# Kernel tuning notes

Measured on AMD Instinct MI355X. Metric: run time of the kernel, lower is better.

Reference implementation:

```python
import jax, jax.numpy as jnp
import numpy as np
from jax import lax

B, C_IN, D, H, W = 1, 64, 48, 48, 48
R = 3
PC = 64          # proj_channels
OC = 128         # out_channels
K = (2 * R + 1) ** 3  # 343 offsets
OFFSETS = np.array([(dz, dy, dx)
                    for dz in range(-R, R + 1)
                    for dy in range(-R, R + 1)
                    for dx in range(-R, R + 1)], dtype=np.int32)


def setup_inputs() -> dict:
    key = jax.random.key(0)
    ks = jax.random.split(key, 10)
    s = 0.05
    return {
        'source_features': jax.random.normal(ks[0], (B, C_IN, D, H, W), jnp.float32),
        'warped_target_features': jax.random.normal(ks[1], (B, C_IN, D, H, W), jnp.float32),
        'proj_src_w': jax.random.normal(ks[2], (PC, C_IN, 1, 1, 1), jnp.float32) * s,
        'proj_src_b': jax.random.normal(ks[3], (PC,), jnp.float32) * s,
        'proj_tgt_w': jax.random.normal(ks[4], (PC, C_IN, 1, 1, 1), jnp.float32) * s,
        'proj_tgt_b': jax.random.normal(ks[5], (PC,), jnp.float32) * s,
        'enc1_w': jax.random.normal(ks[6], (OC, K + 3, 3, 3, 3), jnp.float32) * s,
        'enc1_b': jax.random.normal(ks[7], (OC,), jnp.float32) * s,
        'enc2_w': jax.random.normal(ks[8], (OC, OC, 3, 3, 3), jnp.float32) * s,
        'enc2_b': jax.random.normal(ks[9], (OC,), jnp.float32) * s,
    }


def conv3d(x, w, b, pad):
    out = lax.conv_general_dilated(
        x, w, window_strides=(1, 1, 1), padding=[(pad, pad)] * 3,
        dimension_numbers=('NCDHW', 'OIDHW', 'NCDHW'))
    return out + b[None, :, None, None, None]


def l2norm_c(x):
    # torch F.normalize(dim=1): x / max(||x||_2, 1e-12)
    n = jnp.sqrt(jnp.sum(x * x, axis=1, keepdims=True))
    return x / jnp.maximum(n, 1e-12)


def instance_norm(x, eps=1e-5):
    # InstanceNorm3d, affine=False: per (B,C), biased var over D,H,W
    m = jnp.mean(x, axis=(2, 3, 4), keepdims=True)
    v = jnp.var(x, axis=(2, 3, 4), keepdims=True)
    return (x - m) * lax.rsqrt(v + eps)


def reference(source_features, warped_target_features,
              proj_src_w, proj_src_b, proj_tgt_w, proj_tgt_b,
              enc1_w, enc1_b, enc2_w, enc2_b):
    sp = l2norm_c(conv3d(source_features, proj_src_w, proj_src_b, 0))
    tp = l2norm_c(conv3d(warped_target_features, proj_tgt_w, proj_tgt_b, 0))
    padded = jnp.pad(tp, ((0, 0), (0, 0), (R, R), (R, R), (R, R)), mode='edge')
    offs = jnp.asarray(OFFSETS)  # [K,3] int32

    def corr_one(off):
        # shifted window of padded target, dot over channels -> [B,D,H,W]
        shifted = lax.dynamic_slice(
            padded, (0, 0, R + off[0], R + off[1], R + off[2]), sp.shape)
        return jnp.sum(sp * shifted, axis=1)

    corr = lax.map(corr_one, offs)          # [K,B,D,H,W]
    corr = jnp.moveaxis(corr, 0, 1)         # [B,K,D,H,W]

    # online-softmax expected offset == softmax over K weighted by offset vecs
    wts = jax.nn.softmax(corr, axis=1)
    eo = jnp.einsum('bkdhw,kc->bcdhw', wts, offs.astype(sp.dtype))  # [B,3,D,H,W]

    feat = jnp.concatenate([corr, eo], axis=1)  # [B,K+3,D,H,W]
    h = conv3d(feat, enc1_w, enc1_b, 1)
    h = jax.nn.gelu(instance_norm(h), approximate=False)
    h = conv3d(h, enc2_w, enc2_b, 1)
    h = jax.nn.gelu(instance_norm(h), approximate=False)
    return h
```

## Files before the change

### kernel.cpp

```cpp
#include <hip/hip_runtime.h>
#include <math.h>
#include <stdint.h>

#define VOL 110592
#define CINP 64
#define PCH 64

typedef short short8 __attribute__((ext_vector_type(8)));
typedef float floatx4 __attribute__((ext_vector_type(4)));
typedef _Float16 h8 __attribute__((ext_vector_type(8)));
typedef _Float16 h2v __attribute__((ext_vector_type(2)));

__device__ __forceinline__ ushort f2bf(float f) {
    union { float f; uint32_t u; } v; v.f = f;
    uint32_t r = v.u + 0x7FFFu + ((v.u >> 16) & 1u);
    return (ushort)(r >> 16);
}

__device__ __forceinline__ float hdot2(h2v a, h2v b, float c) {
#if __has_builtin(__builtin_amdgcn_fdot2)
    return __builtin_amdgcn_fdot2(a, b, c, false);
#else
    return fmaf((float)a[0], (float)b[0], fmaf((float)a[1], (float)b[1], c));
#endif
}

__global__ __launch_bounds__(256) void proj_l2norm_kernel(
    const float* __restrict__ x,
    const float* __restrict__ w,
    const float* __restrict__ b,
    _Float16* __restrict__ out)
{
    const int v = blockIdx.x * 256 + threadIdx.x;
    float xr[CINP];
    for (int ci = 0; ci < CINP; ci++)
        xr[ci] = x[(size_t)ci * VOL + v];

    float acc[PCH];
    for (int c = 0; c < PCH; c++) {
        float a = b[c];
        #pragma unroll
        for (int ci = 0; ci < CINP; ci++)
            a = fmaf(w[c * CINP + ci], xr[ci], a);
        acc[c] = a;
    }
    float s = 0.f;
    #pragma unroll
    for (int c = 0; c < PCH; c++) s += acc[c] * acc[c];
    const float inv = 1.0f / fmaxf(sqrtf(s), 1e-12f);
    #pragma unroll
    for (int c = 0; c < PCH; c++)
        out[(size_t)v * PCH + c] = (_Float16)(acc[c] * inv);
}

__global__ __launch_bounds__(256) void corr_fused_kernel(
    const _Float16* __restrict__ sp,
    const _Float16* __restrict__ tp,
    ushort* __restrict__ featT)
{
    const int t  = threadIdx.x;
    const int c8 = t & 7;
    const int vg = t >> 3;
    const int v  = blockIdx.x * 32 + vg;
    const int x = v % 48, y = (v / 48) % 48, z = v / 2304;

    __shared__ __align__(16) ushort lds[32 * 360];

    const h8 s = *(const h8*)(sp + (size_t)v * PCH + c8 * 8);

    const bool owner = (c8 < 7);
    const float fdx_own = (float)(c8 - 3);
    float ssum = 0.f, e0 = 0.f, e1 = 0.f;

    int k = 0;
    for (int dz = -3; dz <= 3; dz++) {
        const int zb = min(max(z + dz, 0), 47) * 2304;
        const float fdz = (float)dz;
        for (int dy = -3; dy <= 3; dy++) {
            const int rb = zb + min(max(y + dy, 0), 47) * 48;
            const float fdy = (float)dy;
            h8 tv[7];
            #pragma unroll
            for (int dxi = 0; dxi < 7; dxi++) {
                const int xc = min(max(x + dxi - 3, 0), 47);
                tv[dxi] = *(const h8*)(tp + (size_t)(rb + xc) * PCH + c8 * 8);
            }
            float p[8];
            #pragma unroll
            for (int dxi = 0; dxi < 7; dxi++) {
                const h8 tvv = tv[dxi];
                float d0 = hdot2((h2v){s[0], s[1]}, (h2v){tvv[0], tvv[1]}, 0.f);
                d0 = hdot2((h2v){s[2], s[3]}, (h2v){tvv[2], tvv[3]}, d0);
                float d1 = hdot2((h2v){s[4], s[5]}, (h2v){tvv[4], tvv[5]}, 0.f);
                d1 = hdot2((h2v){s[6], s[7]}, (h2v){tvv[6], tvv[7]}, d1);
                p[dxi] = d0 + d1;
            }
            p[7] = 0.f;

            float r0, r1, r2, r3;
            {
                const bool hi = (c8 & 1);
                float m0 = hi ? p[0] : p[1];
                float m1 = hi ? p[2] : p[3];
                float m2 = hi ? p[4] : p[5];
                float m3 = hi ? p[6] : p[7];
                m0 = __shfl_xor(m0, 1);
                m1 = __shfl_xor(m1, 1);
                m2 = __shfl_xor(m2, 1);
                m3 = __shfl_xor(m3, 1);
                r0 = (hi ? p[1] : p[0]) + m0;
                r1 = (hi ? p[3] : p[2]) + m1;
                r2 = (hi ? p[5] : p[4]) + m2;
                r3 = (hi ? p[7] : p[6]) + m3;
            }
            float q0, q1;
            {
                const bool hi = (c8 & 2);
                float m0 = hi ? r0 : r1;
                float m1 = hi ? r2 : r3;
                m0 = __shfl_xor(m0, 2);
                m1 = __shfl_xor(m1, 2);
                q0 = (hi ? r1 : r0) + m0;
                q1 = (hi ? r3 : r2) + m1;
            }
            float dot;
            {
                const bool hi = (c8 & 4);
                float m0 = hi ? q0 : q1;
                m0 = __shfl_xor(m0, 4);
                dot = (hi ? q1 : q0) + m0;
            }

            if (owner) {
                lds[vg * 360 + k + c8] = f2bf(dot);
                const float e = __expf(dot);
                ssum += e;
                e0 = fmaf(e, fdz, e0);
                e1 = fmaf(e, fdy, e1);
            }
            k += 7;
        }
    }

    float e2 = fdx_own * ssum;
    #pragma unroll
    for (int m = 1; m < 8; m <<= 1) {
        ssum += __shfl_xor(ssum, m);
        e0   += __shfl_xor(e0, m);
        e1   += __shfl_xor(e1, m);
        e2   += __shfl_xor(e2, m);
    }

    if (c8 == 0) {
        const float inv = 1.f / ssum;
        lds[vg * 360 + 343] = f2bf(e0 * inv);
        lds[vg * 360 + 344] = f2bf(e1 * inv);
        lds[vg * 360 + 345] = f2bf(e2 * inv);
        #pragma unroll
        for (int j = 346; j < 352; j++) lds[vg * 360 + j] = 0;
    }
    __syncthreads();

    ushort* ob = featT + (size_t)blockIdx.x * 32 * 352;
    #pragma unroll
    for (int j = 0; j < 6; j++) {
        const int idx = t + j * 256;
        if (idx < 1408) {
            const int row = idx / 44, col = (idx % 44) * 8;
            *(int4*)(ob + (size_t)row * 352 + col) = *(const int4*)(&lds[row * 360 + col]);
        }
    }
}

template<int CIN, int CPAD>
__global__ __launch_bounds__(256) void wprep_kernel(
    const float* __restrict__ w, ushort* __restrict__ wTo, float* __restrict__ zp)
{
    if (blockIdx.x == 0 && threadIdx.x < 4) zp[threadIdx.x] = 0.f;
    const int oc = blockIdx.x;
    for (int idx = threadIdx.x; idx < CPAD * 27; idx += 256) {
        const int icp = idx / 27, tap = idx - icp * 27;
        float val = 0.f;
        if (icp < CIN) val = w[((size_t)oc * CIN + icp) * 27 + tap];
        wTo[((size_t)tap * 128 + oc) * CPAD + icp] = f2bf(val);
    }
}

template<int CPAD>
__global__ __launch_bounds__(256, 4) void conv3_mfma_kernel(
    const ushort* __restrict__ xT,
    const ushort* __restrict__ wT,
    const float* __restrict__ bias,
    const ushort* __restrict__ zpad,
    float* __restrict__ out)
{
    const int blk = (blockIdx.x % 8) * 108 + (blockIdx.x / 8);
    const int tx = blk % 3, ty = (blk / 3) % 12, tz = blk / 36;
    const int x0 = tx * 16, y0 = ty * 4, z0 = tz * 2;
    const int t = threadIdx.x;
    const int wave = t >> 6;
    const int lane = t & 63;
    const int l = lane & 15;
    const int q = lane >> 4;
    const int ocw = (wave & 1) * 64;
    const int mzw = wave >> 1;

    __shared__ __align__(16) ushort win[432 * 32];

    int off[7];
    #pragma unroll
    for (int it = 0; it < 7; it++) {
        const int c = wave + it * 4;
        off[it] = -1;
        if (c < 27) {
            const int i = c * 64 + lane;
            const int p = i >> 2, g = i & 3;
            const int wz = p / 108, pr = p - wz * 108;
            const int wy = pr / 18, wx = pr - wy * 18;
            const int gz = z0 + wz - 1, gy = y0 + wy - 1, gx = x0 + wx - 1;
            if ((unsigned)gx < 48u && (unsigned)gy < 48u && (unsigned)gz < 48u)
                off[it] = ((gz * 2304 + gy * 48 + gx) * CPAD + g * 8) * 2;
        }
    }

    floatx4 acc[4][4];
    #pragma unroll
    for (int i = 0; i < 4; i++)
        #pragma unroll
        for (int j = 0; j < 4; j++)
            acc[i][j] = (floatx4){0.f, 0.f, 0.f, 0.f};

    const ushort* wbase = wT + (size_t)(ocw + l) * CPAD + q * 8;
    const int ldsbase = (mzw * 108 + l) * 32 + q * 8;

    const int NCH = CPAD / 32;
    #pragma unroll 1
    for (int ck = 0; ck < NCH; ck++) {
        if (ck) __syncthreads();

        const char* xck = (const char*)xT + (size_t)ck * 64;
        #pragma unroll
        for (int it = 0; it < 7; it++) {
            const int c = wave + it * 4;
            if (c < 27) {
                const ushort* gp = (off[it] >= 0)
                    ? (const ushort*)(xck + off[it])
                    : zpad;
                __builtin_amdgcn_global_load_lds(
                    (const __attribute__((address_space(1))) uint32_t*)gp,
                    (__attribute__((address_space(3))) uint32_t*)(win + c * 512 + lane * 8),
                    16, 0, 0);
            }
        }

        const ushort* wck = wbase + ck * 32;
        short8 A0[4], A1[4];
        A0[0] = *(const short8*)(wck);
        A0[1] = *(const short8*)(wck + 16 * CPAD);
        A0[2] = *(const short8*)(wck + 32 * CPAD);
        A0[3] = *(const short8*)(wck + 48 * CPAD);

        __syncthreads();

#define CONV_BODY(TP, AU, AL)                                              \
        {                                                                  \
            const int tpn_ = (TP) + 1;                                     \
            if (tpn_ < 27) {                                               \
                const ushort* wp_ = wck + (size_t)tpn_ * (128 * CPAD);     \
                AL[0] = *(const short8*)(wp_);                             \
                AL[1] = *(const short8*)(wp_ + 16 * CPAD);                 \
                AL[2] = *(const short8*)(wp_ + 32 * CPAD);                 \
                AL[3] = *(const short8*)(wp_ + 48 * CPAD);                 \
            }                                                              \
            const int dz_ = (TP) / 9;                                      \
            const int dy_ = ((TP) / 3) % 3;                                \
            const int dx_ = (TP) % 3;                                      \
            const int pb_ = ldsbase + (dz_ * 108 + dy_ * 18 + dx_) * 32;   \
            const short8 b0_ = *(const short8*)(&win[pb_ +    0]);         \
            const short8 b1_ = *(const short8*)(&win[pb_ +  576]);         \
            const short8 b2_ = *(const short8*)(&win[pb_ + 1152]);         \
            const short8 b3_ = *(const short8*)(&win[pb_ + 1728]);         \
            acc[0][0] = __builtin_amdgcn_mfma_f32_16x16x32_bf16(AU[0], b0_, acc[0][0], 0, 0, 0); \
            acc[1][0] = __builtin_amdgcn_mfma_f32_16x16x32_bf16(AU[1], b0_, acc[1][0], 0, 0, 0); \
            acc[2][0] = __builtin_amdgcn_mfma_f32_16x16x32_bf16(AU[2], b0_, acc[2][0], 0, 0, 0); \
            acc[3][0] = __builtin_amdgcn_mfma_f32_16x16x32_bf16(AU[3], b0_, acc[3][0], 0, 0, 0); \
            acc[0][1] = __builtin_amdgcn_mfma_f32_16x16x32_bf16(AU[0], b1_, acc[0][1], 0, 0, 0); \
            acc[1][1] = __builtin_amdgcn_mfma_f32_16x16x32_bf16(AU[1], b1_, acc[1][1], 0, 0, 0); \
            acc[2][1] = __builtin_amdgcn_mfma_f32_16x16x32_bf16(AU[2], b1_, acc[2][1], 0, 0, 0); \
            acc[3][1] = __builtin_amdgcn_mfma_f32_16x16x32_bf16(AU[3], b1_, acc[3][1], 0, 0, 0); \
            acc[0][2] = __builtin_amdgcn_mfma_f32_16x16x32_bf16(AU[0], b2_, acc[0][2], 0, 0, 0); \
            acc[1][2] = __builtin_amdgcn_mfma_f32_16x16x32_bf16(AU[1], b2_, acc[1][2], 0, 0, 0); \
            acc[2][2] = __builtin_amdgcn_mfma_f32_16x16x32_bf16(AU[2], b2_, acc[2][2], 0, 0, 0); \
            acc[3][2] = __builtin_amdgcn_mfma_f32_16x16x32_bf16(AU[3], b2_, acc[3][2], 0, 0, 0); \
            acc[0][3] = __builtin_amdgcn_mfma_f32_16x16x32_bf16(AU[0], b3_, acc[0][3], 0, 0, 0); \
            acc[1][3] = __builtin_amdgcn_mfma_f32_16x16x32_bf16(AU[1], b3_, acc[1][3], 0, 0, 0); \
            acc[2][3] = __builtin_amdgcn_mfma_f32_16x16x32_bf16(AU[2], b3_, acc[2][3], 0, 0, 0); \
            acc[3][3] = __builtin_amdgcn_mfma_f32_16x16x32_bf16(AU[3], b3_, acc[3][3], 0, 0, 0); \
        }

        #pragma unroll 1
        for (int tg = 0; tg < 13; tg++) {
            const int tp = tg * 2;
            CONV_BODY(tp, A0, A1);
            CONV_BODY(tp + 1, A1, A0);
        }
        CONV_BODY(26, A0, A1);
#undef CONV_BODY
    }

    #pragma unroll
    for (int nt = 0; nt < 4; nt++) {
        const int ocb = ocw + nt * 16 + q * 4;
        const float4 bv = *(const float4*)(bias + ocb);
        #pragma unroll
        for (int mt = 0; mt < 4; mt++) {
            const int v = (z0 + mzw) * 2304 + (y0 + mt) * 48 + x0 + l;
            out[(size_t)(ocb + 0) * VOL + v] = acc[nt][mt][0] + bv.x;
            out[(size_t)(ocb + 1) * VOL + v] = acc[nt][mt][1] + bv.y;
            out[(size_t)(ocb + 2) * VOL + v] = acc[nt][mt][2] + bv.z;
            out[(size_t)(ocb + 3) * VOL + v] = acc[nt][mt][3] + bv.w;
        }
    }
}

__global__ __launch_bounds__(256) void chan_stats_part_kernel(
    const float* __restrict__ x, float* __restrict__ pstats )
{
    const int c = blockIdx.x, g = blockIdx.y;
    const float4* p = (const float4*)(x + (size_t)c * VOL) + g * 3456;
    float s = 0.f, s2 = 0.f;
    #pragma unroll
    for (int j = 0; j < 14; j++) {
        const int i = threadIdx.x + j * 256;
        if (i < 3456) {
            const float4 v = p[i];
            s += v.x + v.y + v.z + v.w;
            s2 = fmaf(v.x, v.x, fmaf(v.y, v.y, fmaf(v.z, v.z, fmaf(v.w, v.w, s2))));
        }
    }
    s  += __shfl_down(s, 32);  s  += __shfl_down(s, 16);
    s  += __shfl_down(s, 8);   s  += __shfl_down(s, 4);
    s  += __shfl_down(s, 2);   s  += __shfl_down(s, 1);
    s2 += __shfl_down(s2, 32); s2 += __shfl_down(s2, 16);
    s2 += __shfl_down(s2, 8);  s2 += __shfl_down(s2, 4);
    s2 += __shfl_down(s2, 2);  s2 += __shfl_down(s2, 1);
    __shared__ float rs[4], rs2[4];
    if ((threadIdx.x & 63) == 0) {
        rs[threadIdx.x >> 6] = s;
        rs2[threadIdx.x >> 6] = s2;
    }
    __syncthreads();
    if (threadIdx.x == 0) {
        pstats[(c * 8 + g) * 2]     = rs[0] + rs[1] + rs[2] + rs[3];
        pstats[(c * 8 + g) * 2 + 1] = rs2[0] + rs2[1] + rs2[2] + rs2[3];
    }
}

__global__ __launch_bounds__(128) void chan_stats_fin_kernel(
    const float* __restrict__ pstats, float* __restrict__ stats )
{
    const int c = threadIdx.x;
    float s = 0.f, s2 = 0.f;
    #pragma unroll
    for (int g = 0; g < 8; g++) {
        s  += pstats[(c * 8 + g) * 2];
        s2 += pstats[(c * 8 + g) * 2 + 1];
    }
    const float mean = s / (float)VOL;
    const float var  = s2 / (float)VOL - mean * mean;
    stats[c * 2]     = mean;
    stats[c * 2 + 1] = rsqrtf(var + 1e-5f);
}

__device__ __forceinline__ float gelu_exact(float h)
{
    return 0.5f * h * (1.f + erff(h * 0.70710678118654752f));
}

__global__ __launch_bounds__(256) void norm_gelu_kernel(
    const float* __restrict__ x, const float* __restrict__ stats,
    float* __restrict__ out)
{
    const size_t i = (size_t)blockIdx.x * 256 + threadIdx.x;
    const int c = (int)(i / (VOL / 4));
    const float mean = stats[c * 2], rstd = stats[c * 2 + 1];
    const float4 xv = ((const float4*)x)[i];
    float4 o;
    o.x = gelu_exact((xv.x - mean) * rstd);
    o.y = gelu_exact((xv.y - mean) * rstd);
    o.z = gelu_exact((xv.z - mean) * rstd);
    o.w = gelu_exact((xv.w - mean) * rstd);
    ((float4*)out)[i] = o;
}

__global__ __launch_bounds__(256) void norm_gelu_transpose_kernel(
    const float* __restrict__ x, const float* __restrict__ stats,
    ushort* __restrict__ outT)
{
    __shared__ float tile[32][33];
    const int v0 = blockIdx.x * 32;
    const int c0 = blockIdx.y * 32;
    const int t = threadIdx.x;
    const int vl = t & 31, cl = t >> 5;
    #pragma unroll
    for (int i = 0; i < 4; i++) {
        const int c = c0 + cl + i * 8;
        const float mean = stats[c * 2], rstd = stats[c * 2 + 1];
        const float val = x[(size_t)c * VOL + v0 + vl];
        tile[cl + i * 8][vl] = gelu_exact((val - mean) * rstd);
    }
    __syncthreads();
    const int vw = t >> 3, cg = t & 7;
    ushort4 o;
    o.x = f2bf(tile[cg * 4 + 0][vw]);
    o.y = f2bf(tile[cg * 4 + 1][vw]);
    o.z = f2bf(tile[cg * 4 + 2][vw]);
    o.w = f2bf(tile[cg * 4 + 3][vw]);
    *(ushort4*)(outT + (size_t)(v0 + vw) * 128 + c0 + cg * 4) = o;
}

extern "C" void kernel_launch(void* const* d_in, const int* in_sizes, int n_in,
                              void* d_out, int out_size, void* d_ws, size_t ws_size,
                              hipStream_t stream)
{
    const float* src = (const float*)d_in[0];
    const float* tgt = (const float*)d_in[1];
    const float* psw = (const float*)d_in[2];
    const float* psb = (const float*)d_in[3];
    const float* ptw = (const float*)d_in[4];
    const float* ptb = (const float*)d_in[5];
    const float* e1w = (const float*)d_in[6];
    const float* e1b = (const float*)d_in[7];
    const float* e2w = (const float*)d_in[8];
    const float* e2b = (const float*)d_in[9];

    float* ws = (float*)d_ws;
    _Float16* sp  = (_Float16*)ws;
    _Float16* tp  = (_Float16*)(ws + (size_t)32 * VOL);
    ushort* featT = (ushort*)(ws + (size_t)128 * VOL);
    float*  h1    = ws;
    float*  h2    = ws + (size_t)128 * VOL;
    ushort* h1T   = (ushort*)(ws + (size_t)304 * VOL);
    float*  w1Tf  = ws + (size_t)368 * VOL;
    ushort* w1T   = (ushort*)w1Tf;
    float*  w2Tf  = w1Tf + 608256;
    ushort* w2T   = (ushort*)w2Tf;
    float*  stats = w2Tf + 221184;
    float*  pstats = stats + 256;
    float*  zpadf  = pstats + 2048;
    const ushort* zpad = (const ushort*)zpadf;

    wprep_kernel<346, 352><<<128, 256, 0, stream>>>(e1w, w1T, zpadf);
    wprep_kernel<128, 128><<<128, 256, 0, stream>>>(e2w, w2T, zpadf);

    proj_l2norm_kernel<<<432, 256, 0, stream>>>(src, psw, psb, sp);
    proj_l2norm_kernel<<<432, 256, 0, stream>>>(tgt, ptw, ptb, tp);
    corr_fused_kernel<<<3456, 256, 0, stream>>>(sp, tp, featT);

    conv3_mfma_kernel<352><<<864, 256, 0, stream>>>(featT, w1T, e1b, zpad, h1);
    chan_stats_part_kernel<<<dim3(128, 8), 256, 0, stream>>>(h1, pstats);
    chan_stats_fin_kernel<<<1, 128, 0, stream>>>(pstats, stats);
    norm_gelu_transpose_kernel<<<dim3(3456, 4), 256, 0, stream>>>(h1, stats, h1T);

    conv3_mfma_kernel<128><<<864, 256, 0, stream>>>(h1T, w2T, e2b, zpad, h2);
    chan_stats_part_kernel<<<dim3(128, 8), 256, 0, stream>>>(h2, pstats);
    chan_stats_fin_kernel<<<1, 128, 0, stream>>>(pstats, stats);
    norm_gelu_kernel<<<(128 * VOL) / 1024, 256, 0, stream>>>(h2, stats, (float*)d_out);
}
```

Measured before the change: 1.026 ms.

## Double-buffer LDS input window and prefetch B fragments in conv3 MFMA kernel

```diff
diff --git a/kernel.cpp b/kernel.cpp
--- a/kernel.cpp
+++ b/kernel.cpp
@@ -187,7 +187,7 @@
 }
 
 template<int CPAD>
-__global__ __launch_bounds__(256, 4) void conv3_mfma_kernel(
+__global__ __launch_bounds__(256, 2) void conv3_mfma_kernel(
     const ushort* __restrict__ xT,
     const ushort* __restrict__ wT,
     const float* __restrict__ bias,
@@ -205,7 +205,7 @@
     const int ocw = (wave & 1) * 64;
     const int mzw = wave >> 1;
 
-    __shared__ __align__(16) ushort win[432 * 32];
+    __shared__ __align__(16) ushort win[2][432 * 32];
 
     int off[7];
     #pragma unroll
@@ -233,36 +233,49 @@
     const ushort* wbase = wT + (size_t)(ocw + l) * CPAD + q * 8;
     const int ldsbase = (mzw * 108 + l) * 32 + q * 8;
 
+#define STAGE(CK, BUFP)                                                    \
+    {                                                                      \
+        const char* xck_ = (const char*)xT + (size_t)(CK) * 64;            \
+        _Pragma("unroll")                                                  \
+        for (int it_ = 0; it_ < 7; it_++) {                                \
+            const int c_ = wave + it_ * 4;                                 \
+            if (c_ < 27) {                                                 \
+                const ushort* gp_ = (off[it_] >= 0)                        \
+                    ? (const ushort*)(xck_ + off[it_]) : zpad;             \
+                __builtin_amdgcn_global_load_lds(                          \
+                    (const __attribute__((address_space(1))) uint32_t*)gp_,\
+                    (__attribute__((address_space(3))) uint32_t*)((BUFP) + c_ * 512 + lane * 8), \
+                    16, 0, 0);                                             \
+            }                                                              \
+        }                                                                  \
+    }
+
     const int NCH = CPAD / 32;
+
+    STAGE(0, &win[0][0]);
+    __syncthreads();
+
     #pragma unroll 1
     for (int ck = 0; ck < NCH; ck++) {
-        if (ck) __syncthreads();
-
-        const char* xck = (const char*)xT + (size_t)ck * 64;
-        #pragma unroll
-        for (int it = 0; it < 7; it++) {
-            const int c = wave + it * 4;
-            if (c < 27) {
-                const ushort* gp = (off[it] >= 0)
-                    ? (const ushort*)(xck + off[it])
-                    : zpad;
-                __builtin_amdgcn_global_load_lds(
-                    (const __attribute__((address_space(1))) uint32_t*)gp,
-                    (__attribute__((address_space(3))) uint32_t*)(win + c * 512 + lane * 8),
-                    16, 0, 0);
-            }
-        }
-
+        const ushort* cbuf = &win[ck & 1][0];
+        ushort* nbuf = &win[(ck + 1) & 1][0];
         const ushort* wck = wbase + ck * 32;
+
         short8 A0[4], A1[4];
         A0[0] = *(const short8*)(wck);
         A0[1] = *(const short8*)(wck + 16 * CPAD);
         A0[2] = *(const short8*)(wck + 32 * CPAD);
         A0[3] = *(const short8*)(wck + 48 * CPAD);
 
-        __syncthreads();
-
-#define CONV_BODY(TP, AU, AL)                                              \
+        short8 B0[4], B1[4];
+        B0[0] = *(const short8*)(&cbuf[ldsbase +    0]);
+        B0[1] = *(const short8*)(&cbuf[ldsbase +  576]);
+        B0[2] = *(const short8*)(&cbuf[ldsbase + 1152]);
+        B0[3] = *(const short8*)(&cbuf[ldsbase + 1728]);
+
+        if (ck + 1 < NCH) STAGE(ck + 1, nbuf);
+
+#define CONV_BODY(TP, AU, AL, BU, BL)                                      \
         {                                                                  \
             const int tpn_ = (TP) + 1;                                     \
             if (tpn_ < 27) {                                               \
@@ -271,42 +284,45 @@
                 AL[1] = *(const short8*)(wp_ + 16 * CPAD);                 \
                 AL[2] = *(const short8*)(wp_ + 32 * CPAD);                 \
                 AL[3] = *(const short8*)(wp_ + 48 * CPAD);                 \
+                const int dzn_ = tpn_ / 9;                                 \
+                const int dyn_ = (tpn_ / 3) % 3;                           \
+                const int dxn_ = tpn_ % 3;                                 \
+                const int pbn_ = ldsbase + (dzn_ * 108 + dyn_ * 18 + dxn_) * 32; \
+                BL[0] = *(const short8*)(&cbuf[pbn_ +    0]);              \
+                BL[1] = *(const short8*)(&cbuf[pbn_ +  576]);              \
+                BL[2] = *(const short8*)(&cbuf[pbn_ + 1152]);              \
+                BL[3] = *(const short8*)(&cbuf[pbn_ + 1728]);              \
             }                                                              \
-            const int dz_ = (TP) / 9;                                      \
-            const int dy_ = ((TP) / 3) % 3;                                \
-            const int dx_ = (TP) % 3;                                      \
-            const int pb_ = ldsbase + (dz_ * 108 + dy_ * 18 + dx_) * 32;   \
-            const short8 b0_ = *(const short8*)(&win[pb_ +    0]);         \
-            const short8 b1_ = *(const short8*)(&win[pb_ +  576]);         \
-            const short8 b2_ = *(const short8*)(&win[pb_ + 1152]);         \
-            const short8 b3_ = *(const short8*)(&win[pb_ + 1728]);         \
-            acc[0][0] = __builtin_amdgcn_mfma_f32_16x16x32_bf16(AU[0], b0_, acc[0][0], 0, 0, 0); \
-            acc[1][0] = __builtin_amdgcn_mfma_f32_16x16x32_bf16(AU[1], b0_, acc[1][0], 0, 0, 0); \
-            acc[2][0] = __builtin_amdgcn_mfma_f32_16x16x32_bf16(AU[2], b0_, acc[2][0], 0, 0, 0); \
-            acc[3][0] = __builtin_amdgcn_mfma_f32_16x16x32_bf16(AU[3], b0_, acc[3][0], 0, 0, 0); \
-            acc[0][1] = __builtin_amdgcn_mfma_f32_16x16x32_bf16(AU[0], b1_, acc[0][1], 0, 0, 0); \
-            acc[1][1] = __builtin_amdgcn_mfma_f32_16x16x32_bf16(AU[1], b1_, acc[1][1], 0, 0, 0); \
-            acc[2][1] = __builtin_amdgcn_mfma_f32_16x16x32_bf16(AU[2], b1_, acc[2][1], 0, 0, 0); \
-            acc[3][1] = __builtin_amdgcn_mfma_f32_16x16x32_bf16(AU[3], b1_, acc[3][1], 0, 0, 0); \
-            acc[0][2] = __builtin_amdgcn_mfma_f32_16x16x32_bf16(AU[0], b2_, acc[0][2], 0, 0, 0); \
-            acc[1][2] = __builtin_amdgcn_mfma_f32_16x16x32_bf16(AU[1], b2_, acc[1][2], 0, 0, 0); \
-            acc[2][2] = __builtin_amdgcn_mfma_f32_16x16x32_bf16(AU[2], b2_, acc[2][2], 0, 0, 0); \
-            acc[3][2] = __builtin_amdgcn_mfma_f32_16x16x32_bf16(AU[3], b2_, acc[3][2], 0, 0, 0); \
-            acc[0][3] = __builtin_amdgcn_mfma_f32_16x16x32_bf16(AU[0], b3_, acc[0][3], 0, 0, 0); \
-            acc[1][3] = __builtin_amdgcn_mfma_f32_16x16x32_bf16(AU[1], b3_, acc[1][3], 0, 0, 0); \
-            acc[2][3] = __builtin_amdgcn_mfma_f32_16x16x32_bf16(AU[2], b3_, acc[2][3], 0, 0, 0); \
-            acc[3][3] = __builtin_amdgcn_mfma_f32_16x16x32_bf16(AU[3], b3_, acc[3][3], 0, 0, 0); \
+            acc[0][0] = __builtin_amdgcn_mfma_f32_16x16x32_bf16(AU[0], BU[0], acc[0][0], 0, 0, 0); \
+            acc[1][0] = __builtin_amdgcn_mfma_f32_16x16x32_bf16(AU[1], BU[0], acc[1][0], 0, 0, 0); \
+            acc[2][0] = __builtin_amdgcn_mfma_f32_16x16x32_bf16(AU[2], BU[0], acc[2][0], 0, 0, 0); \
+            acc[3][0] = __builtin_amdgcn_mfma_f32_16x16x32_bf16(AU[3], BU[0], acc[3][0], 0, 0, 0); \
+            acc[0][1] = __builtin_amdgcn_mfma_f32_16x16x32_bf16(AU[0], BU[1], acc[0][1], 0, 0, 0); \
+            acc[1][1] = __builtin_amdgcn_mfma_f32_16x16x32_bf16(AU[1], BU[1], acc[1][1], 0, 0, 0); \
+            acc[2][1] = __builtin_amdgcn_mfma_f32_16x16x32_bf16(AU[2], BU[1], acc[2][1], 0, 0, 0); \
+            acc[3][1] = __builtin_amdgcn_mfma_f32_16x16x32_bf16(AU[3], BU[1], acc[3][1], 0, 0, 0); \
+            acc[0][2] = __builtin_amdgcn_mfma_f32_16x16x32_bf16(AU[0], BU[2], acc[0][2], 0, 0, 0); \
+            acc[1][2] = __builtin_amdgcn_mfma_f32_16x16x32_bf16(AU[1], BU[2], acc[1][2], 0, 0, 0); \
+            acc[2][2] = __builtin_amdgcn_mfma_f32_16x16x32_bf16(AU[2], BU[2], acc[2][2], 0, 0, 0); \
+            acc[3][2] = __builtin_amdgcn_mfma_f32_16x16x32_bf16(AU[3], BU[2], acc[3][2], 0, 0, 0); \
+            acc[0][3] = __builtin_amdgcn_mfma_f32_16x16x32_bf16(AU[0], BU[3], acc[0][3], 0, 0, 0); \
+            acc[1][3] = __builtin_amdgcn_mfma_f32_16x16x32_bf16(AU[1], BU[3], acc[1][3], 0, 0, 0); \
+            acc[2][3] = __builtin_amdgcn_mfma_f32_16x16x32_bf16(AU[2], BU[3], acc[2][3], 0, 0, 0); \
+            acc[3][3] = __builtin_amdgcn_mfma_f32_16x16x32_bf16(AU[3], BU[3], acc[3][3], 0, 0, 0); \
         }
 
         #pragma unroll 1
         for (int tg = 0; tg < 13; tg++) {
             const int tp = tg * 2;
-            CONV_BODY(tp, A0, A1);
-            CONV_BODY(tp + 1, A1, A0);
-        }
-        CONV_BODY(26, A0, A1);
+            CONV_BODY(tp, A0, A1, B0, B1);
+            CONV_BODY(tp + 1, A1, A0, B1, B0);
+        }
+        CONV_BODY(26, A0, A1, B0, B1);
 #undef CONV_BODY
-    }
+
+        __syncthreads();
+    }
+#undef STAGE
 
     #pragma unroll
     for (int nt = 0; nt < 4; nt++) {
```

Result: no change. 1.019 ms (-0.7%).
